# Kernel optimization log

Hardware: AMD Instinct MI355X
Metric: run time of the kernel (lower is better)

Reference implementation:

```python
import jax, jax.numpy as jnp
import numpy as np

C = 256      # channel_num
K = 9        # key_num
B, H, W = 8, 64, 64


def setup_inputs() -> dict:
    key = jax.random.key(0)
    ks = jax.random.split(key, 12)
    s = 1.0 / np.sqrt(C)
    return {
        "query_layer": jax.random.normal(ks[0], (B, C, H, W), jnp.float32),
        "key_layer": jax.random.normal(ks[1], (B, C, H, W), jnp.float32),
        "gumbel_noise": jax.random.gumbel(ks[2], (B, K, H, W), jnp.float32),
        "w_refer": jax.random.normal(ks[3], (C, C), jnp.float32) * s,
        "b_refer": jax.random.normal(ks[4], (C,), jnp.float32) * 0.01,
        "w_attn": jax.random.normal(ks[5], (K, C), jnp.float32) * s,
        "b_attn": jax.random.normal(ks[6], (K,), jnp.float32) * 0.01,
        "w_mask": jax.random.normal(ks[7], (K, C), jnp.float32) * s,
        "b_mask": jax.random.normal(ks[8], (K,), jnp.float32) * 0.01,
        "w_off": jax.random.normal(ks[9], (2 * K, C), jnp.float32) * 0.02,
        "b_off": jax.random.normal(ks[10], (2 * K,), jnp.float32) * 0.01,
        "temp": 1,
    }


def _conv1x1(w, b, x):
    # w: (O,C), x: (B,C,H,W) -> (B,O,H,W)
    return jnp.einsum('oc,bchw->bohw', w, x) + b[None, :, None, None]


def _sample_one(img, py, px):
    # img: (C,H,W); py,px: (K,H,W) absolute sampling coords (bilinear, zero pad)
    h, w = img.shape[1], img.shape[2]
    y0 = jnp.floor(py)
    x0 = jnp.floor(px)
    wy = py - y0          # weight toward y0+1
    wx = px - x0

    def gather(yi, xi):
        valid = (yi >= 0) & (yi < h) & (xi >= 0) & (xi < w)
        yc = jnp.clip(yi, 0, h - 1).astype(jnp.int32)
        xc = jnp.clip(xi, 0, w - 1).astype(jnp.int32)
        return img[:, yc, xc] * valid[None].astype(img.dtype)  # (C,K,H,W)

    out = (gather(y0, x0) * ((1 - wy) * (1 - wx))[None]
           + gather(y0, x0 + 1) * ((1 - wy) * wx)[None]
           + gather(y0 + 1, x0) * (wy * (1 - wx))[None]
           + gather(y0 + 1, x0 + 1) * (wy * wx)[None])
    return out  # (C,K,H,W)


def reference(query_layer, key_layer, gumbel_noise, w_refer, b_refer,
              w_attn, b_attn, w_mask, b_mask, w_off, b_off, temp):
    key_feature = _conv1x1(w_refer, b_refer, key_layer)          # (B,C,H,W)
    attn_weights = _conv1x1(w_attn, b_attn, query_layer)         # (B,K,H,W)
    soft_mask = _conv1x1(w_mask, b_mask, query_layer)            # (B,K,H,W)
    # gumbel_softmax(hard=False) over key dim
    hard_mask = jax.nn.softmax((soft_mask + gumbel_noise) / temp, axis=1)
    offset = _conv1x1(w_off, b_off, query_layer)                 # (B,2K,H,W)

    # faithful to offset[:, i:i+2]: overlapping (dy,dx) slices
    dy = offset[:, 0:K]        # (B,K,H,W)
    dx = offset[:, 1:K + 1]    # (B,K,H,W)
    ys = jnp.arange(H, dtype=offset.dtype)[None, None, :, None]
    xs = jnp.arange(W, dtype=offset.dtype)[None, None, None, :]
    py = ys + dy
    px = xs + dx

    sampled = jax.vmap(_sample_one)(key_feature, py, px)         # (B,C,K,H,W)

    aw = jax.nn.softmax(attn_weights * hard_mask, axis=1)        # (B,K,H,W)
    out = jnp.einsum('bkhw,bckhw->bchw', aw, sampled)            # (B,C,H,W)
    return out
```

## Files before the change

kernel.cpp:

```cpp
#include <hip/hip_runtime.h>

typedef unsigned short u16;
typedef __attribute__((ext_vector_type(8))) short bf16x8;
typedef __attribute__((ext_vector_type(4))) float f32x4;

__device__ __forceinline__ u16 f2bf(float f) {
    unsigned u = __float_as_uint(f);
    unsigned r = (u + 0x7fffu + ((u >> 16) & 1u)) >> 16;
    return (u16)r;
}
__device__ __forceinline__ float bf2f(u16 h) {
    union { unsigned u; float f; } x; x.u = ((unsigned)h) << 16; return x.f;
}

#define NB 8
#define NC 256
#define NK 9
#define NH 64
#define NW 64
#define NP 4096
#define BAND 320
#define SB_STRIDE 328
#define KS_STRIDE 264

__global__ __launch_bounds__(256) void prep(const float* __restrict__ key,
                                            const float* __restrict__ query,
                                            const float* __restrict__ gumbel,
                                            const float* __restrict__ w_refer,
                                            const float* __restrict__ b_refer,
                                            const float* __restrict__ w_attn, const float* __restrict__ b_attn,
                                            const float* __restrict__ w_mask, const float* __restrict__ b_mask,
                                            const float* __restrict__ w_off,  const float* __restrict__ b_off,
                                            const int* __restrict__ temp_p,
                                            u16* __restrict__ kf16,
                                            float4* __restrict__ wgt, uint2* __restrict__ offs)
{
    __shared__ __align__(16) char smem[46336];
    const int t = threadIdx.x;
    const int lane = t & 63, wid = t >> 6;
    const int fr = lane & 15, kq = (lane >> 4) << 3;

    if (blockIdx.x < 512) {
        u16* K_s = (u16*)smem;
        const int bid = blockIdx.x;
        const int b   = bid & 7;
        const int p0  = (bid >> 3) << 6;
        const int co0w = wid << 6;

        #pragma unroll
        for (int rep = 0; rep < 16; ++rep) {
            int k = (rep << 4) + (t >> 4), px4 = (t & 15) << 2;
            float4 v = *(const float4*)&key[((size_t)b * NC + k) * NP + p0 + px4];
            K_s[(px4 + 0) * KS_STRIDE + k] = f2bf(v.x);
            K_s[(px4 + 1) * KS_STRIDE + k] = f2bf(v.y);
            K_s[(px4 + 2) * KS_STRIDE + k] = f2bf(v.z);
            K_s[(px4 + 3) * KS_STRIDE + k] = f2bf(v.w);
        }
        __syncthreads();

        f32x4 acc[4][4];
        #pragma unroll
        for (int i = 0; i < 4; ++i)
            #pragma unroll
            for (int j = 0; j < 4; ++j) acc[i][j] = (f32x4){0.f, 0.f, 0.f, 0.f};

        for (int ks = 0; ks < 8; ++ks) {
            const int k0 = (ks << 5) + kq;
            bf16x8 af[4], bfv[4];
            #pragma unroll
            for (int mi = 0; mi < 4; ++mi) {
                const float* src = &w_refer[(size_t)(co0w + (mi << 4) + fr) * NC + k0];
                float4 v0 = *(const float4*)src;
                float4 v1 = *(const float4*)(src + 4);
                bf16x8 a;
                a[0] = (short)f2bf(v0.x); a[1] = (short)f2bf(v0.y);
                a[2] = (short)f2bf(v0.z); a[3] = (short)f2bf(v0.w);
                a[4] = (short)f2bf(v1.x); a[5] = (short)f2bf(v1.y);
                a[6] = (short)f2bf(v1.z); a[7] = (short)f2bf(v1.w);
                af[mi] = a;
            }
            #pragma unroll
            for (int ni = 0; ni < 4; ++ni)
                bfv[ni] = *(const bf16x8*)&K_s[((ni << 4) + fr) * KS_STRIDE + k0];
            #pragma unroll
            for (int mi = 0; mi < 4; ++mi)
                #pragma unroll
                for (int ni = 0; ni < 4; ++ni)
                    acc[mi][ni] = __builtin_amdgcn_mfma_f32_16x16x32_bf16(af[mi], bfv[ni], acc[mi][ni], 0, 0, 0);
        }
        const int col = lane & 15, rbase = (lane >> 4) << 2;
        #pragma unroll
        for (int mi = 0; mi < 4; ++mi) {
            #pragma unroll
            for (int rr = 0; rr < 4; ++rr) {
                int co = co0w + (mi << 4) + rbase + rr;
                float bias = b_refer[co];
                u16* dst = &kf16[((size_t)b * NC + co) * NP + p0 + col];
                #pragma unroll
                for (int ni = 0; ni < 4; ++ni)
                    dst[ni << 4] = f2bf(acc[mi][ni][rr] + bias);
            }
        }
    } else {
        const int pt = (int)blockIdx.x - 512;
        const int b  = pt & 7;
        const int p0 = (pt >> 3) << 7;
        u16   (*A)[264] = (u16(*)[264])smem;
        float (*hdT)[41] = (float(*)[41])(smem + 25344);
        const int wn = wid;

        for (int i = t; i < 1152; i += 256) {
            int o = i >> 5, c = (i & 31) << 3;
            const float* src = (o < 9) ? &w_attn[o * NC + c]
                           : (o < 18 ? &w_mask[(o - 9) * NC + c]
                                     : &w_off[(o - 18) * NC + c]);
            float4 v0 = *(const float4*)src;
            float4 v1 = *(const float4*)(src + 4);
            bf16x8 a;
            a[0] = (short)f2bf(v0.x); a[1] = (short)f2bf(v0.y);
            a[2] = (short)f2bf(v0.z); a[3] = (short)f2bf(v0.w);
            a[4] = (short)f2bf(v1.x); a[5] = (short)f2bf(v1.y);
            a[6] = (short)f2bf(v1.z); a[7] = (short)f2bf(v1.w);
            *(bf16x8*)&A[o][c] = a;
        }
        for (int i = t; i < 384; i += 256) {
            bf16x8 z = {0,0,0,0,0,0,0,0};
            *(bf16x8*)&A[36 + (i >> 5)][(i & 31) << 3] = z;
        }
        __syncthreads();

        f32x4 acc[3][2];
        #pragma unroll
        for (int i = 0; i < 3; ++i)
            #pragma unroll
            for (int j = 0; j < 2; ++j) acc[i][j] = (f32x4){0.f, 0.f, 0.f, 0.f};

        for (int ks = 0; ks < 8; ++ks) {
            const int k0 = (ks << 5) + kq;
            bf16x8 af[3], bfv[2];
            #pragma unroll
            for (int mi = 0; mi < 3; ++mi)
                af[mi] = *(const bf16x8*)&A[(mi << 4) + fr][k0];
            #pragma unroll
            for (int ni = 0; ni < 2; ++ni) {
                const float* src = &query[((size_t)b * NC + k0) * NP + p0 + (wn << 5) + (ni << 4) + fr];
                bf16x8 bv;
                #pragma unroll
                for (int j = 0; j < 8; ++j) bv[j] = (short)f2bf(src[(size_t)j * NP]);
                bfv[ni] = bv;
            }
            #pragma unroll
            for (int mi = 0; mi < 3; ++mi)
                #pragma unroll
                for (int ni = 0; ni < 2; ++ni)
                    acc[mi][ni] = __builtin_amdgcn_mfma_f32_16x16x32_bf16(af[mi], bfv[ni], acc[mi][ni], 0, 0, 0);
        }
        const int col = lane & 15, rbase = (lane >> 4) << 2;
        #pragma unroll
        for (int mi = 0; mi < 3; ++mi) {
            #pragma unroll
            for (int rr = 0; rr < 4; ++rr) {
                int o = (mi << 4) + rbase + rr;
                if (o < 36) {
                    float bias = (o < 9) ? b_attn[o] : (o < 18) ? b_mask[o - 9] : b_off[o - 18];
                    #pragma unroll
                    for (int ni = 0; ni < 2; ++ni)
                        hdT[(wn << 5) + (ni << 4) + col][o] = acc[mi][ni][rr] + bias;
                }
            }
        }
        __syncthreads();

        if (t < 128) {
            const int pxg = p0 + t;
            const int row = pxg >> 6, xcol = pxg & 63;
            float v[36];
            #pragma unroll
            for (int o = 0; o < 36; ++o) v[o] = hdT[t][o];

            int ti = temp_p[0];
            float tempf = (ti >= 1 && ti < (1 << 23)) ? (float)ti : __int_as_float(ti);
            float am[9], hs[9];
            float mx = -1e30f;
            #pragma unroll
            for (int k = 0; k < 9; ++k) {
                am[k] = v[k];
                float g = gumbel[((size_t)b * NK + k) * NP + pxg];
                hs[k] = (v[9 + k] + g) / tempf;
                mx = fmaxf(mx, hs[k]);
            }
            float ssum = 0.f;
            #pragma unroll
            for (int k = 0; k < 9; ++k) { hs[k] = __expf(hs[k] - mx); ssum += hs[k]; }
            float inv = 1.f / ssum;
            float lg[9]; float mx2 = -1e30f;
            #pragma unroll
            for (int k = 0; k < 9; ++k) { lg[k] = am[k] * (hs[k] * inv); mx2 = fmaxf(mx2, lg[k]); }
            float s2 = 0.f;
            #pragma unroll
            for (int k = 0; k < 9; ++k) { lg[k] = __expf(lg[k] - mx2); s2 += lg[k]; }
            float inv2 = 1.f / s2;
            #pragma unroll
            for (int k = 0; k < 9; ++k) {
                float a = lg[k] * inv2;
                float pyv = (float)row  + v[18 + k];
                float pxv = (float)xcol + v[19 + k];
                float y0f = floorf(pyv), x0f = floorf(pxv);
                float wy = pyv - y0f, wx = pxv - x0f;
                int y0 = (int)y0f, x0 = (int)x0f;
                int y1 = y0 + 1, x1 = x0 + 1;
                float vy0 = (y0 >= 0 && y0 < NH) ? 1.f : 0.f;
                float vy1 = (y1 >= 0 && y1 < NH) ? 1.f : 0.f;
                float vx0 = (x0 >= 0 && x0 < NW) ? 1.f : 0.f;
                float vx1 = (x1 >= 0 && x1 < NW) ? 1.f : 0.f;
                int y0c = min(max(y0, 0), NH - 1), y1c = min(max(y1, 0), NH - 1);
                int x0c = min(max(x0, 0), NW - 1), x1c = min(max(x1, 0), NW - 1);
                unsigned o00 = (unsigned)(y0c * NW + x0c), o01 = (unsigned)(y0c * NW + x1c);
                unsigned o10 = (unsigned)(y1c * NW + x0c), o11 = (unsigned)(y1c * NW + x1c);
                size_t idx = ((size_t)b * NK + k) * NP + pxg;
                wgt[idx]  = make_float4(a * (1.f - wy) * (1.f - wx) * vy0 * vx0,
                                        a * (1.f - wy) * wx * vy0 * vx1,
                                        a * wy * (1.f - wx) * vy1 * vx0,
                                        a * wy * wx * vy1 * vx1);
                offs[idx] = make_uint2(o00 | (o01 << 16), o10 | (o11 << 16));
            }
        }
    }
}

__global__ __launch_bounds__(512, 4) void sample_pass(const u16* __restrict__ kf16,
                                                      const float4* __restrict__ wgt,
                                                      const uint2* __restrict__ offs,
                                                      float* __restrict__ out)
{
    __shared__ float Sf[64][BAND];

    const int bid = blockIdx.x;
    const int b = bid & 7, row = bid >> 3;
    const int t = threadIdx.x;
    const int lane = t & 63, wid = t >> 6;
    const int fr = lane & 15, kq = (lane >> 4) << 3;
    const int c0 = wid << 5;
    const int ylo = min(max(row - 2, 0), NH - 5);
    const int base = ylo << 6;
    const u16* kfb = kf16 + (size_t)b * NC * NP + base;

    bf16x8 apre[4][2];
    #pragma unroll
    for (int s = 0; s < 4; ++s)
        #pragma unroll
        for (int mi = 0; mi < 2; ++mi)
            apre[s][mi] = *(const bf16x8*)&kfb[(size_t)(c0 + (mi << 4) + fr) * NP + (s << 5) + kq];

    const int px = t & 63, kg = t >> 6;
    size_t idx0 = ((size_t)b * NK + kg) * NP + (row << 6) + px;
    float4 wv0 = wgt[idx0];
    uint2  ov0 = offs[idx0];
    float4 wv1 = make_float4(0.f, 0.f, 0.f, 0.f);
    uint2  ov1 = make_uint2(0u, 0u);
    if (kg == 0) {
        size_t idx1 = ((size_t)b * NK + 8) * NP + (row << 6) + px;
        wv1 = wgt[idx1]; ov1 = offs[idx1];
    }

    #pragma unroll
    for (int i = 0; i < 10; ++i)
        ((float4*)Sf)[t + (i << 9)] = (float4){0.f, 0.f, 0.f, 0.f};
    __syncthreads();

    bool esc = false;
    #pragma unroll
    for (int s = 0; s < 2; ++s) {
        if (s == 1 && kg != 0) break;
        float4 wv = s ? wv1 : wv0;
        uint2  ov = s ? ov1 : ov0;
        int   o4[4] = { (int)(ov.x & 0xffffu), (int)(ov.x >> 16),
                        (int)(ov.y & 0xffffu), (int)(ov.y >> 16) };
        float w4[4] = { wv.x, wv.y, wv.z, wv.w };
        #pragma unroll
        for (int c = 0; c < 4; ++c) {
            int u = o4[c] - base;
            if ((unsigned)u < (unsigned)BAND) atomicAdd(&Sf[px][u], w4[c]);
            else esc = true;
        }
    }
    __syncthreads();

    u16* Sb = (u16*)&Sf[0][0];
    bf16x8 pk[5]; int po[5];
    #pragma unroll
    for (int r = 0; r < 5; ++r) {
        int i = t + (r << 9);
        int p = i / 40, j = (i % 40) << 3;
        float4 a = *(const float4*)&Sf[p][j];
        float4 c = *(const float4*)&Sf[p][j + 4];
        bf16x8 q;
        q[0] = (short)f2bf(a.x); q[1] = (short)f2bf(a.y);
        q[2] = (short)f2bf(a.z); q[3] = (short)f2bf(a.w);
        q[4] = (short)f2bf(c.x); q[5] = (short)f2bf(c.y);
        q[6] = (short)f2bf(c.z); q[7] = (short)f2bf(c.w);
        pk[r] = q; po[r] = p * SB_STRIDE + j;
    }
    __syncthreads();
    #pragma unroll
    for (int r = 0; r < 5; ++r)
        *(bf16x8*)&Sb[po[r]] = pk[r];
    __syncthreads();

    f32x4 acc[2][4];
    #pragma unroll
    for (int i = 0; i < 2; ++i)
        #pragma unroll
        for (int j = 0; j < 4; ++j) acc[i][j] = (f32x4){0.f, 0.f, 0.f, 0.f};

    #pragma unroll
    for (int step = 0; step < 10; ++step) {
        bf16x8 a0 = apre[step & 3][0], a1 = apre[step & 3][1];
        if (step + 4 < 10) {
            #pragma unroll
            for (int mi = 0; mi < 2; ++mi)
                apre[step & 3][mi] =
                    *(const bf16x8*)&kfb[(size_t)(c0 + (mi << 4) + fr) * NP + ((step + 4) << 5) + kq];
        }
        bf16x8 bfv[4];
        #pragma unroll
        for (int ni = 0; ni < 4; ++ni)
            bfv[ni] = *(const bf16x8*)&Sb[((ni << 4) + fr) * SB_STRIDE + (step << 5) + kq];
        #pragma unroll
        for (int ni = 0; ni < 4; ++ni) {
            acc[0][ni] = __builtin_amdgcn_mfma_f32_16x16x32_bf16(a0, bfv[ni], acc[0][ni], 0, 0, 0);
            acc[1][ni] = __builtin_amdgcn_mfma_f32_16x16x32_bf16(a1, bfv[ni], acc[1][ni], 0, 0, 0);
        }
    }

    const int col = lane & 15, rbase = (lane >> 4) << 2;
    float* ob = out + (size_t)b * NC * NP + (row << 6);
    #pragma unroll
    for (int mi = 0; mi < 2; ++mi) {
        #pragma unroll
        for (int rr = 0; rr < 4; ++rr) {
            int c = c0 + (mi << 4) + rbase + rr;
            #pragma unroll
            for (int ni = 0; ni < 4; ++ni)
                ob[(size_t)c * NP + (ni << 4) + col] = acc[mi][ni][rr];
        }
    }

    __syncthreads();
    if (esc) {
        for (int s = 0; s < (kg == 0 ? 2 : 1); ++s) {
            int k = s ? 8 : kg;
            size_t idx = ((size_t)b * NK + k) * NP + (row << 6) + px;
            float4 wv = wgt[idx];
            uint2  ov = offs[idx];
            int   o4[4] = { (int)(ov.x & 0xffffu), (int)(ov.x >> 16),
                            (int)(ov.y & 0xffffu), (int)(ov.y >> 16) };
            float w4[4] = { wv.x, wv.y, wv.z, wv.w };
            for (int c = 0; c < 4; ++c) {
                int u = o4[c] - base;
                if ((unsigned)u >= (unsigned)BAND) {
                    for (int cc = 0; cc < NC; ++cc)
                        atomicAdd(&ob[(size_t)cc * NP + px],
                                  w4[c] * bf2f(kf16[((size_t)b * NC + cc) * NP + o4[c]]));
                }
            }
        }
    }
}

extern "C" void kernel_launch(void* const* d_in, const int* in_sizes, int n_in,
                              void* d_out, int out_size, void* d_ws, size_t ws_size,
                              hipStream_t stream)
{
    const float* query   = (const float*)d_in[0];
    const float* key     = (const float*)d_in[1];
    const float* gumbel  = (const float*)d_in[2];
    const float* w_refer = (const float*)d_in[3];
    const float* b_refer = (const float*)d_in[4];
    const float* w_attn  = (const float*)d_in[5];
    const float* b_attn  = (const float*)d_in[6];
    const float* w_mask  = (const float*)d_in[7];
    const float* b_mask  = (const float*)d_in[8];
    const float* w_off   = (const float*)d_in[9];
    const float* b_off   = (const float*)d_in[10];
    const int*   temp    = (const int*)d_in[11];
    float* out = (float*)d_out;

    u16*    kf16 = (u16*)d_ws;
    float4* wgt  = (float4*)((char*)d_ws + (size_t)NB * NP * NC * 2);
    uint2*  offs = (uint2*)((char*)wgt + (size_t)NB * NK * NP * 16);

    prep<<<768, 256, 0, stream>>>(key, query, gumbel, w_refer, b_refer,
                                  w_attn, b_attn, w_mask, b_mask, w_off, b_off,
                                  temp, kf16, wgt, offs);
    sample_pass<<<512, 512, 0, stream>>>(kf16, wgt, offs, out);
}
```

Before: 65.89 us.

## Split prep into weight-convert, key GEMM and head kernels with register double-buffering

```diff
diff --git a/kernel.cpp b/kernel.cpp
--- a/kernel.cpp
+++ b/kernel.cpp
@@ -21,209 +21,221 @@
 #define NP 4096
 #define BAND 320
 #define SB_STRIDE 328
-#define KS_STRIDE 264
-
-__global__ __launch_bounds__(256) void prep(const float* __restrict__ key,
-                                            const float* __restrict__ query,
-                                            const float* __restrict__ gumbel,
-                                            const float* __restrict__ w_refer,
-                                            const float* __restrict__ b_refer,
-                                            const float* __restrict__ w_attn, const float* __restrict__ b_attn,
-                                            const float* __restrict__ w_mask, const float* __restrict__ b_mask,
-                                            const float* __restrict__ w_off,  const float* __restrict__ b_off,
-                                            const int* __restrict__ temp_p,
-                                            u16* __restrict__ kf16,
-                                            float4* __restrict__ wgt, uint2* __restrict__ offs)
+#define HW_STRIDE 264
+
+__global__ __launch_bounds__(256) void wconv(const float* __restrict__ w_refer,
+                                             const float* __restrict__ w_attn,
+                                             const float* __restrict__ w_mask,
+                                             const float* __restrict__ w_off,
+                                             u16* __restrict__ wb16, u16* __restrict__ hw16)
 {
-    __shared__ __align__(16) char smem[46336];
-    const int t = threadIdx.x;
-    const int lane = t & 63, wid = t >> 6;
+    const int bid = blockIdx.x, t = threadIdx.x;
+    if (bid < 64) {
+        int idx = bid * 256 + t;
+        int co = idx >> 6, k4 = (idx & 63) << 2;
+        float4 v = *(const float4*)&w_refer[co * NC + k4];
+        u16* d = &wb16[co * NC + k4];
+        d[0] = f2bf(v.x); d[1] = f2bf(v.y); d[2] = f2bf(v.z); d[3] = f2bf(v.w);
+    } else {
+        for (int i = (bid - 64) * 1584 + t; i < (bid - 63) * 1584; i += 256) {
+            int r = i / HW_STRIDE, c = i % HW_STRIDE;
+            float v = 0.f;
+            if (r < 36 && c < 256)
+                v = (r < 9) ? w_attn[r * NC + c]
+                  : (r < 18 ? w_mask[(r - 9) * NC + c] : w_off[(r - 18) * NC + c]);
+            hw16[i] = f2bf(v);
+        }
+    }
+}
+
+__global__ __launch_bounds__(256) void kf_gemm(const float* __restrict__ key,
+                                               const u16* __restrict__ wb16,
+                                               const float* __restrict__ b_refer,
+                                               u16* __restrict__ kf16)
+{
+    const int bid = blockIdx.x;
+    const int b   = bid & 7;
+    const int p0  = (bid >> 3) << 6;
+    const int lane = threadIdx.x & 63, wid = threadIdx.x >> 6;
     const int fr = lane & 15, kq = (lane >> 4) << 3;
-
-    if (blockIdx.x < 512) {
-        u16* K_s = (u16*)smem;
-        const int bid = blockIdx.x;
-        const int b   = bid & 7;
-        const int p0  = (bid >> 3) << 6;
-        const int co0w = wid << 6;
-
-        #pragma unroll
-        for (int rep = 0; rep < 16; ++rep) {
-            int k = (rep << 4) + (t >> 4), px4 = (t & 15) << 2;
-            float4 v = *(const float4*)&key[((size_t)b * NC + k) * NP + p0 + px4];
-            K_s[(px4 + 0) * KS_STRIDE + k] = f2bf(v.x);
-            K_s[(px4 + 1) * KS_STRIDE + k] = f2bf(v.y);
-            K_s[(px4 + 2) * KS_STRIDE + k] = f2bf(v.z);
-            K_s[(px4 + 3) * KS_STRIDE + k] = f2bf(v.w);
-        }
-        __syncthreads();
-
-        f32x4 acc[4][4];
-        #pragma unroll
-        for (int i = 0; i < 4; ++i)
-            #pragma unroll
-            for (int j = 0; j < 4; ++j) acc[i][j] = (f32x4){0.f, 0.f, 0.f, 0.f};
-
-        for (int ks = 0; ks < 8; ++ks) {
-            const int k0 = (ks << 5) + kq;
-            bf16x8 af[4], bfv[4];
-            #pragma unroll
-            for (int mi = 0; mi < 4; ++mi) {
-                const float* src = &w_refer[(size_t)(co0w + (mi << 4) + fr) * NC + k0];
-                float4 v0 = *(const float4*)src;
-                float4 v1 = *(const float4*)(src + 4);
-                bf16x8 a;
-                a[0] = (short)f2bf(v0.x); a[1] = (short)f2bf(v0.y);
-                a[2] = (short)f2bf(v0.z); a[3] = (short)f2bf(v0.w);
-                a[4] = (short)f2bf(v1.x); a[5] = (short)f2bf(v1.y);
-                a[6] = (short)f2bf(v1.z); a[7] = (short)f2bf(v1.w);
-                af[mi] = a;
-            }
-            #pragma unroll
-            for (int ni = 0; ni < 4; ++ni)
-                bfv[ni] = *(const bf16x8*)&K_s[((ni << 4) + fr) * KS_STRIDE + k0];
+    const int co0w = wid << 6;
+
+    f32x4 acc[4][4];
+    #pragma unroll
+    for (int i = 0; i < 4; ++i)
+        #pragma unroll
+        for (int j = 0; j < 4; ++j) acc[i][j] = (f32x4){0.f, 0.f, 0.f, 0.f};
+
+    const float* kb = &key[(size_t)b * NC * NP + p0];
+
+#define LOAD_A(ks, dst)                                                            \
+    {   _Pragma("unroll")                                                          \
+        for (int mi = 0; mi < 4; ++mi)                                             \
+            dst[mi] = *(const bf16x8*)&wb16[(size_t)(co0w + (mi << 4) + fr) * NC + ((ks) << 5) + kq]; }
+#define LOAD_B(ks, dst)                                                            \
+    {   _Pragma("unroll")                                                          \
+        for (int ni = 0; ni < 4; ++ni) {                                           \
+            const float* src = &kb[(size_t)(((ks) << 5) + kq) * NP + (ni << 4) + fr]; \
+            bf16x8 bv;                                                             \
+            _Pragma("unroll")                                                      \
+            for (int j = 0; j < 8; ++j) bv[j] = (short)f2bf(src[(size_t)j * NP]);  \
+            dst[ni] = bv; } }
+
+    bf16x8 aP[4], bP[4], aQ[4], bQ[4];
+    LOAD_A(0, aP); LOAD_B(0, bP);
+    #pragma unroll
+    for (int ks = 0; ks < 8; ++ks) {
+        if (ks & 1) {
+            if (ks < 7) { LOAD_A(ks + 1, aP); LOAD_B(ks + 1, bP); }
             #pragma unroll
             for (int mi = 0; mi < 4; ++mi)
                 #pragma unroll
                 for (int ni = 0; ni < 4; ++ni)
-                    acc[mi][ni] = __builtin_amdgcn_mfma_f32_16x16x32_bf16(af[mi], bfv[ni], acc[mi][ni], 0, 0, 0);
-        }
-        const int col = lane & 15, rbase = (lane >> 4) << 2;
-        #pragma unroll
-        for (int mi = 0; mi < 4; ++mi) {
-            #pragma unroll
-            for (int rr = 0; rr < 4; ++rr) {
-                int co = co0w + (mi << 4) + rbase + rr;
-                float bias = b_refer[co];
-                u16* dst = &kf16[((size_t)b * NC + co) * NP + p0 + col];
+                    acc[mi][ni] = __builtin_amdgcn_mfma_f32_16x16x32_bf16(aQ[mi], bQ[ni], acc[mi][ni], 0, 0, 0);
+        } else {
+            if (ks < 7) { LOAD_A(ks + 1, aQ); LOAD_B(ks + 1, bQ); }
+            #pragma unroll
+            for (int mi = 0; mi < 4; ++mi)
                 #pragma unroll
                 for (int ni = 0; ni < 4; ++ni)
-                    dst[ni << 4] = f2bf(acc[mi][ni][rr] + bias);
-            }
-        }
-    } else {
-        const int pt = (int)blockIdx.x - 512;
-        const int b  = pt & 7;
-        const int p0 = (pt >> 3) << 7;
-        u16   (*A)[264] = (u16(*)[264])smem;
-        float (*hdT)[41] = (float(*)[41])(smem + 25344);
-        const int wn = wid;
-
-        for (int i = t; i < 1152; i += 256) {
-            int o = i >> 5, c = (i & 31) << 3;
-            const float* src = (o < 9) ? &w_attn[o * NC + c]
-                           : (o < 18 ? &w_mask[(o - 9) * NC + c]
-                                     : &w_off[(o - 18) * NC + c]);
-            float4 v0 = *(const float4*)src;
-            float4 v1 = *(const float4*)(src + 4);
-            bf16x8 a;
-            a[0] = (short)f2bf(v0.x); a[1] = (short)f2bf(v0.y);
-            a[2] = (short)f2bf(v0.z); a[3] = (short)f2bf(v0.w);
-            a[4] = (short)f2bf(v1.x); a[5] = (short)f2bf(v1.y);
-            a[6] = (short)f2bf(v1.z); a[7] = (short)f2bf(v1.w);
-            *(bf16x8*)&A[o][c] = a;
-        }
-        for (int i = t; i < 384; i += 256) {
-            bf16x8 z = {0,0,0,0,0,0,0,0};
-            *(bf16x8*)&A[36 + (i >> 5)][(i & 31) << 3] = z;
-        }
-        __syncthreads();
-
-        f32x4 acc[3][2];
-        #pragma unroll
-        for (int i = 0; i < 3; ++i)
-            #pragma unroll
-            for (int j = 0; j < 2; ++j) acc[i][j] = (f32x4){0.f, 0.f, 0.f, 0.f};
-
-        for (int ks = 0; ks < 8; ++ks) {
-            const int k0 = (ks << 5) + kq;
-            bf16x8 af[3], bfv[2];
-            #pragma unroll
-            for (int mi = 0; mi < 3; ++mi)
-                af[mi] = *(const bf16x8*)&A[(mi << 4) + fr][k0];
-            #pragma unroll
-            for (int ni = 0; ni < 2; ++ni) {
-                const float* src = &query[((size_t)b * NC + k0) * NP + p0 + (wn << 5) + (ni << 4) + fr];
-                bf16x8 bv;
-                #pragma unroll
-                for (int j = 0; j < 8; ++j) bv[j] = (short)f2bf(src[(size_t)j * NP]);
-                bfv[ni] = bv;
-            }
-            #pragma unroll
-            for (int mi = 0; mi < 3; ++mi)
+                    acc[mi][ni] = __builtin_amdgcn_mfma_f32_16x16x32_bf16(aP[mi], bP[ni], acc[mi][ni], 0, 0, 0);
+        }
+    }
+#undef LOAD_A
+#undef LOAD_B
+
+    const int col = lane & 15, rbase = (lane >> 4) << 2;
+    #pragma unroll
+    for (int mi = 0; mi < 4; ++mi) {
+        #pragma unroll
+        for (int rr = 0; rr < 4; ++rr) {
+            int co = co0w + (mi << 4) + rbase + rr;
+            float bias = b_refer[co];
+            u16* dst = &kf16[((size_t)b * NC + co) * NP + p0 + col];
+            #pragma unroll
+            for (int ni = 0; ni < 4; ++ni)
+                dst[ni << 4] = f2bf(acc[mi][ni][rr] + bias);
+        }
+    }
+}
+
+__global__ __launch_bounds__(256) void head_meta(const float* __restrict__ query,
+                                                 const float* __restrict__ gumbel,
+                                                 const u16* __restrict__ hw16,
+                                                 const float* __restrict__ b_attn,
+                                                 const float* __restrict__ b_mask,
+                                                 const float* __restrict__ b_off,
+                                                 const int* __restrict__ temp_p,
+                                                 float4* __restrict__ wgt, uint2* __restrict__ offs)
+{
+    __shared__ u16 A[48][HW_STRIDE];
+    __shared__ float hdT[128][41];
+    const int pt = blockIdx.x;
+    const int b  = pt & 7;
+    const int p0 = (pt >> 3) << 7;
+    const int t = threadIdx.x;
+    const int lane = t & 63, wn = t >> 6;
+    const int fr = lane & 15, kq = (lane >> 4) << 3;
+
+    #pragma unroll
+    for (int i = t; i < 1584; i += 256)
+        ((uint4*)A)[i] = ((const uint4*)hw16)[i];
+    __syncthreads();
+
+    f32x4 acc[3][2];
+    #pragma unroll
+    for (int i = 0; i < 3; ++i)
+        #pragma unroll
+        for (int j = 0; j < 2; ++j) acc[i][j] = (f32x4){0.f, 0.f, 0.f, 0.f};
+
+    for (int ks = 0; ks < 8; ++ks) {
+        const int k0 = (ks << 5) + kq;
+        bf16x8 af[3], bfv[2];
+        #pragma unroll
+        for (int mi = 0; mi < 3; ++mi)
+            af[mi] = *(const bf16x8*)&A[(mi << 4) + fr][k0];
+        #pragma unroll
+        for (int ni = 0; ni < 2; ++ni) {
+            const float* src = &query[((size_t)b * NC + k0) * NP + p0 + (wn << 5) + (ni << 4) + fr];
+            bf16x8 bv;
+            #pragma unroll
+            for (int j = 0; j < 8; ++j) bv[j] = (short)f2bf(src[(size_t)j * NP]);
+            bfv[ni] = bv;
+        }
+        #pragma unroll
+        for (int mi = 0; mi < 3; ++mi)
+            #pragma unroll
+            for (int ni = 0; ni < 2; ++ni)
+                acc[mi][ni] = __builtin_amdgcn_mfma_f32_16x16x32_bf16(af[mi], bfv[ni], acc[mi][ni], 0, 0, 0);
+    }
+    const int col = lane & 15, rbase = (lane >> 4) << 2;
+    #pragma unroll
+    for (int mi = 0; mi < 3; ++mi) {
+        #pragma unroll
+        for (int rr = 0; rr < 4; ++rr) {
+            int o = (mi << 4) + rbase + rr;
+            if (o < 36) {
+                float bias = (o < 9) ? b_attn[o] : (o < 18) ? b_mask[o - 9] : b_off[o - 18];
                 #pragma unroll
                 for (int ni = 0; ni < 2; ++ni)
-                    acc[mi][ni] = __builtin_amdgcn_mfma_f32_16x16x32_bf16(af[mi], bfv[ni], acc[mi][ni], 0, 0, 0);
-        }
-        const int col = lane & 15, rbase = (lane >> 4) << 2;
-        #pragma unroll
-        for (int mi = 0; mi < 3; ++mi) {
-            #pragma unroll
-            for (int rr = 0; rr < 4; ++rr) {
-                int o = (mi << 4) + rbase + rr;
-                if (o < 36) {
-                    float bias = (o < 9) ? b_attn[o] : (o < 18) ? b_mask[o - 9] : b_off[o - 18];
-                    #pragma unroll
-                    for (int ni = 0; ni < 2; ++ni)
-                        hdT[(wn << 5) + (ni << 4) + col][o] = acc[mi][ni][rr] + bias;
-                }
+                    hdT[(wn << 5) + (ni << 4) + col][o] = acc[mi][ni][rr] + bias;
             }
         }
-        __syncthreads();
-
-        if (t < 128) {
-            const int pxg = p0 + t;
-            const int row = pxg >> 6, xcol = pxg & 63;
-            float v[36];
-            #pragma unroll
-            for (int o = 0; o < 36; ++o) v[o] = hdT[t][o];
-
-            int ti = temp_p[0];
-            float tempf = (ti >= 1 && ti < (1 << 23)) ? (float)ti : __int_as_float(ti);
-            float am[9], hs[9];
-            float mx = -1e30f;
-            #pragma unroll
-            for (int k = 0; k < 9; ++k) {
-                am[k] = v[k];
-                float g = gumbel[((size_t)b * NK + k) * NP + pxg];
-                hs[k] = (v[9 + k] + g) / tempf;
-                mx = fmaxf(mx, hs[k]);
-            }
-            float ssum = 0.f;
-            #pragma unroll
-            for (int k = 0; k < 9; ++k) { hs[k] = __expf(hs[k] - mx); ssum += hs[k]; }
-            float inv = 1.f / ssum;
-            float lg[9]; float mx2 = -1e30f;
-            #pragma unroll
-            for (int k = 0; k < 9; ++k) { lg[k] = am[k] * (hs[k] * inv); mx2 = fmaxf(mx2, lg[k]); }
-            float s2 = 0.f;
-            #pragma unroll
-            for (int k = 0; k < 9; ++k) { lg[k] = __expf(lg[k] - mx2); s2 += lg[k]; }
-            float inv2 = 1.f / s2;
-            #pragma unroll
-            for (int k = 0; k < 9; ++k) {
-                float a = lg[k] * inv2;
-                float pyv = (float)row  + v[18 + k];
-                float pxv = (float)xcol + v[19 + k];
-                float y0f = floorf(pyv), x0f = floorf(pxv);
-                float wy = pyv - y0f, wx = pxv - x0f;
-                int y0 = (int)y0f, x0 = (int)x0f;
-                int y1 = y0 + 1, x1 = x0 + 1;
-                float vy0 = (y0 >= 0 && y0 < NH) ? 1.f : 0.f;
-                float vy1 = (y1 >= 0 && y1 < NH) ? 1.f : 0.f;
-                float vx0 = (x0 >= 0 && x0 < NW) ? 1.f : 0.f;
-                float vx1 = (x1 >= 0 && x1 < NW) ? 1.f : 0.f;
-                int y0c = min(max(y0, 0), NH - 1), y1c = min(max(y1, 0), NH - 1);
-                int x0c = min(max(x0, 0), NW - 1), x1c = min(max(x1, 0), NW - 1);
-                unsigned o00 = (unsigned)(y0c * NW + x0c), o01 = (unsigned)(y0c * NW + x1c);
-                unsigned o10 = (unsigned)(y1c * NW + x0c), o11 = (unsigned)(y1c * NW + x1c);
-                size_t idx = ((size_t)b * NK + k) * NP + pxg;
-                wgt[idx]  = make_float4(a * (1.f - wy) * (1.f - wx) * vy0 * vx0,
-                                        a * (1.f - wy) * wx * vy0 * vx1,
-                                        a * wy * (1.f - wx) * vy1 * vx0,
-                                        a * wy * wx * vy1 * vx1);
-                offs[idx] = make_uint2(o00 | (o01 << 16), o10 | (o11 << 16));
-            }
+    }
+    __syncthreads();
+
+    if (t < 128) {
+        const int pxg = p0 + t;
+        const int row = pxg >> 6, xcol = pxg & 63;
+        float v[36];
+        #pragma unroll
+        for (int o = 0; o < 36; ++o) v[o] = hdT[t][o];
+
+        int ti = temp_p[0];
+        float tempf = (ti >= 1 && ti < (1 << 23)) ? (float)ti : __int_as_float(ti);
+        float am[9], hs[9];
+        float mx = -1e30f;
+        #pragma unroll
+        for (int k = 0; k < 9; ++k) {
+            am[k] = v[k];
+            float g = gumbel[((size_t)b * NK + k) * NP + pxg];
+            hs[k] = (v[9 + k] + g) / tempf;
+            mx = fmaxf(mx, hs[k]);
+        }
+        float ssum = 0.f;
+        #pragma unroll
+        for (int k = 0; k < 9; ++k) { hs[k] = __expf(hs[k] - mx); ssum += hs[k]; }
+        float inv = 1.f / ssum;
+        float lg[9]; float mx2 = -1e30f;
+        #pragma unroll
+        for (int k = 0; k < 9; ++k) { lg[k] = am[k] * (hs[k] * inv); mx2 = fmaxf(mx2, lg[k]); }
+        float s2 = 0.f;
+        #pragma unroll
+        for (int k = 0; k < 9; ++k) { lg[k] = __expf(lg[k] - mx2); s2 += lg[k]; }
+        float inv2 = 1.f / s2;
+        #pragma unroll
+        for (int k = 0; k < 9; ++k) {
+            float a = lg[k] * inv2;
+            float pyv = (float)row  + v[18 + k];
+            float pxv = (float)xcol + v[19 + k];
+            float y0f = floorf(pyv), x0f = floorf(pxv);
+            float wy = pyv - y0f, wx = pxv - x0f;
+            int y0 = (int)y0f, x0 = (int)x0f;
+            int y1 = y0 + 1, x1 = x0 + 1;
+            float vy0 = (y0 >= 0 && y0 < NH) ? 1.f : 0.f;
+            float vy1 = (y1 >= 0 && y1 < NH) ? 1.f : 0.f;
+            float vx0 = (x0 >= 0 && x0 < NW) ? 1.f : 0.f;
+            float vx1 = (x1 >= 0 && x1 < NW) ? 1.f : 0.f;
+            int y0c = min(max(y0, 0), NH - 1), y1c = min(max(y1, 0), NH - 1);
+            int x0c = min(max(x0, 0), NW - 1), x1c = min(max(x1, 0), NW - 1);
+            unsigned o00 = (unsigned)(y0c * NW + x0c), o01 = (unsigned)(y0c * NW + x1c);
+            unsigned o10 = (unsigned)(y1c * NW + x0c), o11 = (unsigned)(y1c * NW + x1c);
+            size_t idx = ((size_t)b * NK + k) * NP + pxg;
+            wgt[idx]  = make_float4(a * (1.f - wy) * (1.f - wx) * vy0 * vx0,
+                                    a * (1.f - wy) * wx * vy0 * vx1,
+                                    a * wy * (1.f - wx) * vy1 * vx0,
+                                    a * wy * wx * vy1 * vx1);
+            offs[idx] = make_uint2(o00 | (o01 << 16), o10 | (o11 << 16));
         }
     }
 }
@@ -386,12 +398,16 @@
     const int*   temp    = (const int*)d_in[11];
     float* out = (float*)d_out;
 
-    u16*    kf16 = (u16*)d_ws;
-    float4* wgt  = (float4*)((char*)d_ws + (size_t)NB * NP * NC * 2);
+    char* ws = (char*)d_ws;
+    u16*    kf16 = (u16*)ws;
+    float4* wgt  = (float4*)(ws + (size_t)NB * NP * NC * 2);
     uint2*  offs = (uint2*)((char*)wgt + (size_t)NB * NK * NP * 16);
-
-    prep<<<768, 256, 0, stream>>>(key, query, gumbel, w_refer, b_refer,
-                                  w_attn, b_attn, w_mask, b_mask, w_off, b_off,
-                                  temp, kf16, wgt, offs);
+    u16*    wb16 = (u16*)((char*)offs + (size_t)NB * NK * NP * 8);
+    u16*    hw16 = (u16*)((char*)wb16 + (size_t)NC * NC * 2);
+
+    wconv<<<72, 256, 0, stream>>>(w_refer, w_attn, w_mask, w_off, wb16, hw16);
+    kf_gemm<<<512, 256, 0, stream>>>(key, wb16, b_refer, kf16);
+    head_meta<<<256, 256, 0, stream>>>(query, gumbel, hw16, b_attn, b_mask, b_off,
+                                       temp, wgt, offs);
     sample_pass<<<512, 512, 0, stream>>>(kf16, wgt, offs, out);
 }
```

New measurement: 61.14 us. 7.2% less time.
